# Kernel optimization log

Hardware: AMD Instinct MI355X
Metric: run time of the kernel (lower is better)

Reference implementation:

```python
import jax, jax.numpy as jnp
import numpy as np

B, T, C = 4, 2048, 1024
H = 16
D = C // H  # head_dim = 64


def setup_inputs() -> dict:
    key = jax.random.key(0)
    k1, k2, k3 = jax.random.split(key, 3)
    scale = 0.02
    x = jax.random.normal(k1, (B, T, C), dtype=jnp.float32)
    w_attn = jax.random.normal(k2, (C, 3 * C), dtype=jnp.float32) * scale
    b_attn = jnp.zeros((3 * C,), dtype=jnp.float32)
    w_proj = jax.random.normal(k3, (C, C), dtype=jnp.float32) * scale
    b_proj = jnp.zeros((C,), dtype=jnp.float32)
    return {"x": x, "w_attn": w_attn, "b_attn": b_attn,
            "w_proj": w_proj, "b_proj": b_proj}


def reference(x, w_attn, b_attn, w_proj, b_proj):
    Bc, Tc, Cc = x.shape
    qkv = x @ w_attn + b_attn                      # [B, T, 3C]
    q, k, v = jnp.split(qkv, 3, axis=-1)
    # [B, H, T, D]
    q = q.reshape(Bc, Tc, H, D).transpose(0, 2, 1, 3)
    k = k.reshape(Bc, Tc, H, D).transpose(0, 2, 1, 3)
    v = v.reshape(Bc, Tc, H, D).transpose(0, 2, 1, 3)
    att = jnp.einsum('bhqd,bhkd->bhqk', q, k) / jnp.sqrt(jnp.float32(D))
    causal = jnp.tril(jnp.ones((Tc, Tc), dtype=bool))
    att = jnp.where(causal, att, -jnp.inf)
    att = jax.nn.softmax(att, axis=-1)
    y = jnp.einsum('bhqk,bhkd->bhqd', att, v)      # [B, H, T, D]
    y = y.transpose(0, 2, 1, 3).reshape(Bc, Tc, Cc)
    return y @ w_proj + b_proj
```

## Files before the change

kernel.cpp:

```cpp
#include <hip/hip_runtime.h>

typedef unsigned short u16;
typedef __bf16 bf16x8 __attribute__((ext_vector_type(8)));
typedef float f32x4 __attribute__((ext_vector_type(4)));

#define T_SEQ 2048
#define NH 16
#define HD 64
#define CDIM 1024

__device__ __forceinline__ u16 f2bf(float f) {
    union { float f; unsigned int u; } v; v.f = f;
    unsigned int r = v.u + 0x7FFFu + ((v.u >> 16) & 1u);
    return (u16)(r >> 16);
}

__device__ __forceinline__ unsigned cvt_pk_bf16(float lo, float hi) {
    unsigned r;
    asm("v_cvt_pk_bf16_f32 %0, %1, %2" : "=v"(r) : "v"(lo), "v"(hi));
    return r;
}

__device__ __forceinline__ void gll16(const u16* g, const u16* l) {
    __builtin_amdgcn_global_load_lds((const __attribute__((address_space(1))) void*)g,
                                     (__attribute__((address_space(3))) void*)l, 16, 0, 0);
}

__global__ void cast_f32_bf16(const float* __restrict__ in, u16* __restrict__ out, int n) {
    int i = (blockIdx.x * blockDim.x + threadIdx.x) * 4;
    if (i >= n) return;
    float4 v = *reinterpret_cast<const float4*>(in + i);
    ushort4 o;
    o.x = f2bf(v.x); o.y = f2bf(v.y); o.z = f2bf(v.z); o.w = f2bf(v.w);
    *reinterpret_cast<ushort4*>(out + i) = o;
}

__global__ void transpose_cast(const float* __restrict__ in, u16* __restrict__ out, int K, int N) {
    __shared__ float tile[32][33];
    int n0 = blockIdx.x * 32, k0 = blockIdx.y * 32;
    int tx = threadIdx.x & 31, ty = threadIdx.x >> 5;
#pragma unroll
    for (int i = 0; i < 32; i += 8)
        tile[ty + i][tx] = in[(size_t)(k0 + ty + i) * N + n0 + tx];
    __syncthreads();
#pragma unroll
    for (int i = 0; i < 32; i += 8)
        out[(size_t)(n0 + ty + i) * K + k0 + tx] = f2bf(tile[tx][ty + i]);
}

template <int EPI>
__global__ __launch_bounds__(256)
void gemm_bt(const u16* __restrict__ A, const u16* __restrict__ Bt,
             const float* __restrict__ bias, float* __restrict__ out,
             u16* __restrict__ qb, u16* __restrict__ kb, u16* __restrict__ vt,
             int M, int N, int K) {
    __shared__ u16 As[128 * 64];
    __shared__ u16 Bs[128 * 64];
    const int tid = threadIdx.x;
    const int lane = tid & 63;
    const int w = tid >> 6;
    const int wm = w >> 1, wn = w & 1;
    const int c = lane & 15, g = lane >> 4;
    const int gm0 = blockIdx.y * 128;
    const int gn0 = blockIdx.x * 128;

    f32x4 acc[4][4] = {};

    for (int k0 = 0; k0 < K; k0 += 64) {
#pragma unroll
        for (int it = 0; it < 4; ++it) {
            int tb = it * 256 + w * 64;
            int task = tb + lane;
            int r = task >> 3, sl = task & 7;
            int sc = sl ^ (r & 7);
            gll16(A + (size_t)(gm0 + r) * K + k0 + sc * 8, As + (size_t)task * 8);
            gll16(Bt + (size_t)(gn0 + r) * K + k0 + sc * 8, Bs + (size_t)task * 8);
        }
        __syncthreads();
#pragma unroll
        for (int kk = 0; kk < 2; ++kk) {
            bf16x8 a[4], b[4];
#pragma unroll
            for (int m = 0; m < 4; ++m) {
                int row = wm * 64 + m * 16 + c;
                a[m] = *reinterpret_cast<const bf16x8*>(&As[row * 64 + (((kk * 4 + g) ^ (c & 7)) * 8)]);
            }
#pragma unroll
            for (int n = 0; n < 4; ++n) {
                int row = wn * 64 + n * 16 + c;
                b[n] = *reinterpret_cast<const bf16x8*>(&Bs[row * 64 + (((kk * 4 + g) ^ (c & 7)) * 8)]);
            }
#pragma unroll
            for (int m = 0; m < 4; ++m)
#pragma unroll
                for (int n = 0; n < 4; ++n)
                    acc[m][n] = __builtin_amdgcn_mfma_f32_16x16x32_bf16(a[m], b[n], acc[m][n], 0, 0, 0);
        }
        __syncthreads();
    }

    if (EPI == 1) {
#pragma unroll
        for (int m = 0; m < 4; ++m)
#pragma unroll
            for (int n = 0; n < 4; ++n) {
                int gcol = gn0 + wn * 64 + n * 16 + c;
                float bv = bias[gcol];
#pragma unroll
                for (int r = 0; r < 4; ++r) {
                    int grow = gm0 + wm * 64 + m * 16 + g * 4 + r;
                    out[(size_t)grow * N + gcol] = acc[m][n][r] + bv;
                }
            }
    } else {
        const int which = gn0 >> 10;
        const int b_ = gm0 >> 11;
        if (which == 2) {
#pragma unroll
            for (int m = 0; m < 4; ++m)
#pragma unroll
                for (int n = 0; n < 4; ++n) {
                    int gcol = gn0 + wn * 64 + n * 16 + c;
                    float bv = bias[gcol];
                    int cc = gcol & 1023;
                    int h = cc >> 6, d = cc & 63;
                    int bh = b_ * NH + h;
                    int t0 = (gm0 & 2047) + wm * 64 + m * 16 + g * 4;
                    ushort4 pk;
                    pk.x = f2bf(acc[m][n][0] + bv);
                    pk.y = f2bf(acc[m][n][1] + bv);
                    pk.z = f2bf(acc[m][n][2] + bv);
                    pk.w = f2bf(acc[m][n][3] + bv);
                    *reinterpret_cast<ushort4*>(&vt[((size_t)bh * HD + d) * T_SEQ + t0]) = pk;
                }
        } else {
            const float qs = (which == 0) ? 0.18033688f : 1.0f;
            u16* dst = (which == 0) ? qb : kb;
#pragma unroll
            for (int m = 0; m < 4; ++m)
#pragma unroll
                for (int n = 0; n < 4; ++n) {
                    int gcol = gn0 + wn * 64 + n * 16 + c;
                    float bv = bias[gcol];
                    int cc = gcol & 1023;
                    int h = cc >> 6, d = cc & 63;
                    int bh = b_ * NH + h;
#pragma unroll
                    for (int r = 0; r < 4; ++r) {
                        int t = (gm0 & 2047) + wm * 64 + m * 16 + g * 4 + r;
                        dst[((size_t)bh * T_SEQ + t) * HD + d] = f2bf((acc[m][n][r] + bv) * qs);
                    }
                }
        }
    }
}

__global__ __launch_bounds__(512, 4)
void attn_fwd(const u16* __restrict__ Qb, const u16* __restrict__ Kb,
              const u16* __restrict__ Vt, u16* __restrict__ yb) {
    __shared__ u16 Ks[2][64 * 64];
    __shared__ u16 Vs[2][64 * 64];
    __shared__ unsigned Ps[8][1024];
    const int tid = threadIdx.x, lane = tid & 63, w = tid >> 6;
    const int g = lane >> 4, c = lane & 15;
    const int f = blockIdx.x;
    const int xcd = f & 7, j = (f >> 3) & 7, bhi = f >> 6;
    const int bh = xcd * 8 + bhi;
    const int b = bh >> 4, hh = bh & 15;
    const float NEG = -1e30f;
    const size_t kBase = (size_t)bh * T_SEQ * HD;
    const size_t vBase = (size_t)bh * HD * T_SEQ;
    unsigned* ps = &Ps[w][0];
    const int sw = c & 7;
    const int qwv[2] = {(15 - j) * 128 + w * 16, j * 128 + w * 16};

    bf16x8 qf[2][2];
#pragma unroll
    for (int u = 0; u < 2; ++u) {
        const u16* qrow = Qb + kBase + (size_t)(qwv[u] + c) * HD;
        qf[u][0] = *reinterpret_cast<const bf16x8*>(qrow + g * 8);
        qf[u][1] = *reinterpret_cast<const bf16x8*>(qrow + 32 + g * 8);
    }

    f32x4 yacc[2][4] = {};
    float l[2] = {0.f, 0.f};
    const int nt = 2 * (15 - j) + 2;
    int cur = 0;

    {
        int r = tid >> 3, sl = tid & 7, sc = sl ^ (r & 7);
        gll16(Kb + kBase + (size_t)r * HD + sc * 8, Ks[0] + (size_t)tid * 8);
        gll16(Vt + vBase + (size_t)r * T_SEQ + sc * 8, Vs[0] + (size_t)tid * 8);
        __syncthreads();
    }

    for (int kt = 0; kt < nt; ++kt) {
        const int kv0 = kt * 64;
        const bool more = (kt + 1 < nt);
        if (more) {
            const int nv0 = kv0 + 64;
            int r = tid >> 3, sl = tid & 7, sc = sl ^ (r & 7);
            gll16(Kb + kBase + (size_t)(nv0 + r) * HD + sc * 8, Ks[cur ^ 1] + (size_t)tid * 8);
            gll16(Vt + vBase + (size_t)r * T_SEQ + nv0 + sc * 8, Vs[cur ^ 1] + (size_t)tid * 8);
        }
        const u16* ks = Ks[cur];
        const u16* vs = Vs[cur];
        const bool a0 = (kv0 <= qwv[0] + 15);
        const bool a1 = (kv0 <= qwv[1] + 15);

        if (a0 || a1) {
            f32x4 s_[2][4];
            __builtin_amdgcn_s_setprio(1);
#pragma unroll
            for (int n = 0; n < 4; ++n) {
                int rb = (n * 16 + c) * 64;
                bf16x8 k0 = *reinterpret_cast<const bf16x8*>(&ks[rb + ((g ^ sw) * 8)]);
                bf16x8 k1 = *reinterpret_cast<const bf16x8*>(&ks[rb + (((4 + g) ^ sw) * 8)]);
                if (a0) {
                    f32x4 t = {};
                    t = __builtin_amdgcn_mfma_f32_16x16x32_bf16(k0, qf[0][0], t, 0, 0, 0);
                    t = __builtin_amdgcn_mfma_f32_16x16x32_bf16(k1, qf[0][1], t, 0, 0, 0);
                    s_[0][n] = t;
                }
                if (a1) {
                    f32x4 t = {};
                    t = __builtin_amdgcn_mfma_f32_16x16x32_bf16(k0, qf[1][0], t, 0, 0, 0);
                    t = __builtin_amdgcn_mfma_f32_16x16x32_bf16(k1, qf[1][1], t, 0, 0, 0);
                    s_[1][n] = t;
                }
            }
            __builtin_amdgcn_s_setprio(0);

            bf16x8 pa[2][2];
#pragma unroll
            for (int u = 0; u < 2; ++u) {
                const bool act = u ? a1 : a0;
                if (act) {
                    const int qwu = qwv[u];
                    if (kv0 + 63 > qwu) {
                        int q = qwu + c;
#pragma unroll
                        for (int n = 0; n < 4; ++n) {
                            int kvb = kv0 + n * 16 + 4 * g;
#pragma unroll
                            for (int r = 0; r < 4; ++r)
                                if (kvb + r > q) s_[u][n][r] = NEG;
                        }
                    }
                    float rsum = 0.f;
                    int base = (16 * u + c) * 32;
#pragma unroll
                    for (int n = 0; n < 4; ++n) {
                        float p0 = __builtin_amdgcn_exp2f(s_[u][n][0]);
                        float p1 = __builtin_amdgcn_exp2f(s_[u][n][1]);
                        float p2 = __builtin_amdgcn_exp2f(s_[u][n][2]);
                        float p3 = __builtin_amdgcn_exp2f(s_[u][n][3]);
                        rsum += (p0 + p1) + (p2 + p3);
                        uint2 pr;
                        pr.x = cvt_pk_bf16(p0, p1);
                        pr.y = cvt_pk_bf16(p2, p3);
                        *reinterpret_cast<uint2*>(&ps[base + ((n ^ (c & 3)) << 3) + 2 * g]) = pr;
                    }
                    l[u] += rsum;
#pragma unroll
                    for (int kk = 0; kk < 2; ++kk) {
                        int idx = (16 * u + c) * 32 + ((kk * 16 + 4 * g) ^ ((c & 3) << 3));
                        pa[u][kk] = *reinterpret_cast<const bf16x8*>(&ps[idx]);
                    }
                }
            }
            __builtin_amdgcn_s_setprio(1);
#pragma unroll
            for (int n = 0; n < 4; ++n) {
                int rb = (n * 16 + c) * 64;
                bf16x8 v0 = *reinterpret_cast<const bf16x8*>(&vs[rb + ((g ^ sw) * 8)]);
                bf16x8 v1 = *reinterpret_cast<const bf16x8*>(&vs[rb + (((4 + g) ^ sw) * 8)]);
                if (a0) {
                    yacc[0][n] = __builtin_amdgcn_mfma_f32_16x16x32_bf16(pa[0][0], v0, yacc[0][n], 0, 0, 0);
                    yacc[0][n] = __builtin_amdgcn_mfma_f32_16x16x32_bf16(pa[0][1], v1, yacc[0][n], 0, 0, 0);
                }
                if (a1) {
                    yacc[1][n] = __builtin_amdgcn_mfma_f32_16x16x32_bf16(pa[1][0], v0, yacc[1][n], 0, 0, 0);
                    yacc[1][n] = __builtin_amdgcn_mfma_f32_16x16x32_bf16(pa[1][1], v1, yacc[1][n], 0, 0, 0);
                }
            }
            __builtin_amdgcn_s_setprio(0);
        }
        if (more) __syncthreads();
        cur ^= 1;
    }
#pragma unroll
    for (int u = 0; u < 2; ++u) {
        float lt = l[u];
        lt += __shfl_xor(lt, 16);
        lt += __shfl_xor(lt, 32);
        float linv = 1.f / lt;
        float lr[4];
#pragma unroll
        for (int r = 0; r < 4; ++r) lr[r] = __shfl(linv, g * 4 + r);
#pragma unroll
        for (int r = 0; r < 4; ++r) {
            int q = qwv[u] + g * 4 + r;
#pragma unroll
            for (int n = 0; n < 4; ++n)
                yb[((size_t)b * T_SEQ + q) * CDIM + hh * HD + n * 16 + c] = f2bf(yacc[u][n][r] * lr[r]);
        }
    }
}

extern "C" void kernel_launch(void* const* d_in, const int* in_sizes, int n_in,
                              void* d_out, int out_size, void* d_ws, size_t ws_size,
                              hipStream_t stream) {
    const float* x      = (const float*)d_in[0];
    const float* w_attn = (const float*)d_in[1];
    const float* b_attn = (const float*)d_in[2];
    const float* w_proj = (const float*)d_in[3];
    const float* b_proj = (const float*)d_in[4];
    float* out = (float*)d_out;

    u16* ws  = (u16*)d_ws;
    u16* xb  = ws;
    u16* wT  = xb  + (size_t)8192 * 1024;
    u16* wpT = wT  + (size_t)3072 * 1024;
    u16* Qb  = wpT + (size_t)1024 * 1024;
    u16* Kb  = Qb  + (size_t)64 * 2048 * 64;
    u16* Vt  = Kb  + (size_t)64 * 2048 * 64;
    u16* yb  = Vt  + (size_t)64 * 2048 * 64;

    cast_f32_bf16<<<8192, 256, 0, stream>>>(x, xb, 8192 * 1024);
    transpose_cast<<<dim3(96, 32), 256, 0, stream>>>(w_attn, wT, 1024, 3072);
    transpose_cast<<<dim3(32, 32), 256, 0, stream>>>(w_proj, wpT, 1024, 1024);
    gemm_bt<0><<<dim3(24, 64), 256, 0, stream>>>(xb, wT, b_attn, nullptr, Qb, Kb, Vt,
                                                 8192, 3072, 1024);
    attn_fwd<<<512, 512, 0, stream>>>(Qb, Kb, Vt, yb);
    gemm_bt<1><<<dim3(8, 64), 256, 0, stream>>>(yb, wpT, b_proj, out, nullptr, nullptr, nullptr,
                                                8192, 1024, 1024);
}
```

Measured before the change: 178.7 us.

## Triple-buffer GEMM LDS loads with 256-row tiles and 512-thread blocks

Restructures the bf16 GEMM into a three-stage LDS pipeline. Tiles for step t+2 are issued via global_load_lds while step t is computed, and each step ends with a single vmcnt-gated barrier instead of two __syncthreads. The block grows to 512 threads covering a 256-row M tile with eight warps, and MFMA sections get raised wave priority. The goal is to hide global-load latency and cut barrier stalls, at the cost of more LDS (about 144KB) and one block per CU.

```diff
diff --git a/kernel.cpp b/kernel.cpp
--- a/kernel.cpp
+++ b/kernel.cpp
@@ -49,54 +49,77 @@
 }
 
 template <int EPI>
-__global__ __launch_bounds__(256)
+__global__ __launch_bounds__(512, 1)
 void gemm_bt(const u16* __restrict__ A, const u16* __restrict__ Bt,
              const float* __restrict__ bias, float* __restrict__ out,
              u16* __restrict__ qb, u16* __restrict__ kb, u16* __restrict__ vt,
              int M, int N, int K) {
-    __shared__ u16 As[128 * 64];
-    __shared__ u16 Bs[128 * 64];
+    __shared__ u16 As[3][256 * 64];
+    __shared__ u16 Bs[3][128 * 64];
     const int tid = threadIdx.x;
     const int lane = tid & 63;
     const int w = tid >> 6;
     const int wm = w >> 1, wn = w & 1;
     const int c = lane & 15, g = lane >> 4;
-    const int gm0 = blockIdx.y * 128;
+    const int gm0 = blockIdx.y * 256;
     const int gn0 = blockIdx.x * 128;
+    const int NT = K >> 6;
 
     f32x4 acc[4][4] = {};
 
-    for (int k0 = 0; k0 < K; k0 += 64) {
+    auto STAGE = [&](int t, int buf) {
+        const int k0 = t << 6;
 #pragma unroll
         for (int it = 0; it < 4; ++it) {
-            int tb = it * 256 + w * 64;
-            int task = tb + lane;
-            int r = task >> 3, sl = task & 7;
-            int sc = sl ^ (r & 7);
-            gll16(A + (size_t)(gm0 + r) * K + k0 + sc * 8, As + (size_t)task * 8);
-            gll16(Bt + (size_t)(gn0 + r) * K + k0 + sc * 8, Bs + (size_t)task * 8);
-        }
-        __syncthreads();
+            int task = tid + it * 512;
+            int r = task >> 3, sl = task & 7, sc = sl ^ (r & 7);
+            gll16(A + (size_t)(gm0 + r) * K + k0 + sc * 8, As[buf] + (size_t)task * 8);
+        }
+#pragma unroll
+        for (int it = 0; it < 2; ++it) {
+            int task = tid + it * 512;
+            int r = task >> 3, sl = task & 7, sc = sl ^ (r & 7);
+            gll16(Bt + (size_t)(gn0 + r) * K + k0 + sc * 8, Bs[buf] + (size_t)task * 8);
+        }
+    };
+
+    STAGE(0, 0);
+    STAGE(1, 1);
+    asm volatile("s_waitcnt vmcnt(6)" ::: "memory");
+    __builtin_amdgcn_s_barrier();
+    asm volatile("" ::: "memory");
+
+    for (int t = 0; t < NT; ++t) {
+        if (t + 2 < NT) STAGE(t + 2, (t + 2) % 3);
+        const u16* as = As[t % 3];
+        const u16* bs = Bs[t % 3];
 #pragma unroll
         for (int kk = 0; kk < 2; ++kk) {
             bf16x8 a[4], b[4];
 #pragma unroll
             for (int m = 0; m < 4; ++m) {
                 int row = wm * 64 + m * 16 + c;
-                a[m] = *reinterpret_cast<const bf16x8*>(&As[row * 64 + (((kk * 4 + g) ^ (c & 7)) * 8)]);
+                a[m] = *reinterpret_cast<const bf16x8*>(&as[row * 64 + (((kk * 4 + g) ^ (c & 7)) * 8)]);
             }
 #pragma unroll
             for (int n = 0; n < 4; ++n) {
                 int row = wn * 64 + n * 16 + c;
-                b[n] = *reinterpret_cast<const bf16x8*>(&Bs[row * 64 + (((kk * 4 + g) ^ (c & 7)) * 8)]);
-            }
+                b[n] = *reinterpret_cast<const bf16x8*>(&bs[row * 64 + (((kk * 4 + g) ^ (c & 7)) * 8)]);
+            }
+            __builtin_amdgcn_s_setprio(1);
 #pragma unroll
             for (int m = 0; m < 4; ++m)
 #pragma unroll
                 for (int n = 0; n < 4; ++n)
                     acc[m][n] = __builtin_amdgcn_mfma_f32_16x16x32_bf16(a[m], b[n], acc[m][n], 0, 0, 0);
-        }
-        __syncthreads();
+            __builtin_amdgcn_s_setprio(0);
+        }
+        if (t + 1 < NT) {
+            if (t + 2 < NT) asm volatile("s_waitcnt vmcnt(6)" ::: "memory");
+            else            asm volatile("s_waitcnt vmcnt(0)" ::: "memory");
+            __builtin_amdgcn_s_barrier();
+            asm volatile("" ::: "memory");
+        }
     }
 
     if (EPI == 1) {
@@ -330,9 +353,9 @@
     cast_f32_bf16<<<8192, 256, 0, stream>>>(x, xb, 8192 * 1024);
     transpose_cast<<<dim3(96, 32), 256, 0, stream>>>(w_attn, wT, 1024, 3072);
     transpose_cast<<<dim3(32, 32), 256, 0, stream>>>(w_proj, wpT, 1024, 1024);
-    gemm_bt<0><<<dim3(24, 64), 256, 0, stream>>>(xb, wT, b_attn, nullptr, Qb, Kb, Vt,
+    gemm_bt<0><<<dim3(24, 32), 512, 0, stream>>>(xb, wT, b_attn, nullptr, Qb, Kb, Vt,
                                                  8192, 3072, 1024);
     attn_fwd<<<512, 512, 0, stream>>>(Qb, Kb, Vt, yb);
-    gemm_bt<1><<<dim3(8, 64), 256, 0, stream>>>(yb, wpT, b_proj, out, nullptr, nullptr, nullptr,
+    gemm_bt<1><<<dim3(8, 32), 512, 0, stream>>>(yb, wpT, b_proj, out, nullptr, nullptr, nullptr,
                                                 8192, 1024, 1024);
 }
```

Result: slower. 187.5 us (+4.9%).
